# Performance work log

Measured on AMD Instinct MI355X. Metric: run time of the kernel, lower is better.

## Reference

```python
import jax, jax.numpy as jnp
import numpy as np

HIDDEN = 512
INPUT = 512


def setup_inputs() -> dict:
    key = jax.random.key(0)
    ks = jax.random.split(key, 13)
    stdv = 1.0 / np.sqrt(HIDDEN)
    u = lambda k, shape: jax.random.uniform(k, shape, jnp.float32, -stdv, stdv)
    inp = {"x": jax.random.normal(ks[0], (64, 1024, INPUT), jnp.float32)}
    names = ["W_i", "U_i", "b_i", "W_f", "U_f", "b_f", "W_c", "U_c", "b_c", "W_o", "U_o", "b_o"]
    shapes = [(INPUT, HIDDEN), (HIDDEN, HIDDEN), (HIDDEN,)] * 4
    for n, s, k in zip(names, shapes, ks[1:]):
        inp[n] = u(k, s)
    return inp


def reference(x, W_i, U_i, b_i, W_f, U_f, b_f, W_c, U_c, b_c, W_o, U_o, b_o):
    bs, seq, _ = x.shape
    hs = U_i.shape[0]
    # Precompute input projections for all timesteps (batched GEMM), then scan the recurrence.
    # Stack 4 gates: [seq, bs, 4*hs]
    W = jnp.concatenate([W_i, W_f, W_c, W_o], axis=1)          # [in, 4h]
    U = jnp.concatenate([U_i, U_f, U_c, U_o], axis=1)          # [h, 4h]
    b = jnp.concatenate([b_i, b_f, b_c, b_o], axis=0)          # [4h]
    x_proj = jnp.einsum('bsi,ih->sbh', x, W) + b               # [seq, bs, 4h]

    def step(carry, xp):
        h, c = carry
        z = xp + h @ U                                          # [bs, 4h]
        i = jax.nn.relu(z[:, 0*hs:1*hs])
        f = jax.nn.relu(z[:, 1*hs:2*hs])
        g = jnp.tanh(z[:, 2*hs:3*hs])
        o = jax.nn.sigmoid(z[:, 3*hs:4*hs])
        c = f * c + i * g
        h = o * jnp.tanh(c)
        return (h, c), h

    h0 = jnp.zeros((bs, hs), x.dtype)
    c0 = jnp.zeros((bs, hs), x.dtype)
    (_, _), hs_seq = jax.lax.scan(step, (h0, c0), x_proj)       # [seq, bs, h]
    return jnp.transpose(hs_seq, (1, 0, 2))                     # [bs, seq, h]
```

## Files before the change

kernel.cpp:

```cpp
#include <hip/hip_runtime.h>
#include <hip/hip_bf16.h>
#include <stdint.h>

typedef float  f32x4  __attribute__((ext_vector_type(4)));
typedef short  bf16x8 __attribute__((ext_vector_type(8)));
typedef unsigned int  u32;
typedef unsigned short u16;
typedef unsigned long long u64;

#define BS    64
#define SEQ   1024
#define HID   512

__device__ __forceinline__ u16 f2bf(float f) {
    u32 u = __float_as_uint(f);
    u32 r = (u + 0x7FFFu + ((u >> 16) & 1u)) >> 16;
    return (u16)r;
}
__device__ __forceinline__ float bf2f(u16 h) {
    return __uint_as_float(((u32)h) << 16);
}
__device__ __forceinline__ u32 pk2(float a, float b) {
    return (u32)f2bf(a) | ((u32)f2bf(b) << 16);
}
__device__ __forceinline__ float sigm(float x)  { return 1.f / (1.f + __expf(-x)); }
__device__ __forceinline__ float tanh_(float x) { return 1.f - 2.f / (1.f + __expf(2.f * x)); }

#define OFF_W4T   0
#define OFF_B4    (2u*1024*1024)
#define OFF_HBUF  (OFF_B4 + 8192)
#define OFF_CBUF  (OFF_HBUF + 262144)
#define OFF_XP    (4u*1024*1024)

__global__ void pack_w(const float* __restrict__ Wi, const float* __restrict__ Wf,
                       const float* __restrict__ Wc, const float* __restrict__ Wo,
                       const float* __restrict__ bi, const float* __restrict__ bf_,
                       const float* __restrict__ bc, const float* __restrict__ bo,
                       u16* __restrict__ w4t, float* __restrict__ b4) {
    int n = blockIdx.x;
    int gate = n >> 9, c = n & 511;
    const float* W = (gate == 0) ? Wi : (gate == 1) ? Wf : (gate == 2) ? Wc : Wo;
    const float* B = (gate == 0) ? bi : (gate == 1) ? bf_ : (gate == 2) ? bc : bo;
    int k = threadIdx.x * 2;
    u32 v = pk2(W[(size_t)k * 512 + c], W[(size_t)(k + 1) * 512 + c]);
    *(u32*)&w4t[(size_t)n * 512 + k] = v;
    if (threadIdx.x == 0) b4[n] = B[c];
}

__global__ __launch_bounds__(256, 2)
void gemm_proj(const float* __restrict__ x, const u16* __restrict__ w4t,
               const float* __restrict__ b4, u16* __restrict__ xp,
               int t0, int Tc) {
    __shared__ __align__(16) u16 lA[128 * 64];
    __shared__ __align__(16) u16 lB[128 * 64];

    int ntb = blockIdx.x & 15;
    int mb  = blockIdx.x >> 4;
    int tps = Tc >> 7;
    int bstrip = mb / tps, tb = mb % tps;
    const float* Abase = x + (size_t)(bstrip * SEQ + t0 + tb * 128) * 512;
    size_t xprow0 = (size_t)bstrip * Tc + tb * 128;
    int n0 = ntb * 128;

    int tid = threadIdx.x, lane = tid & 63, w = tid >> 6;
    int wm = w >> 1, wn = w & 1;

    f32x4 acc[4][4];
#pragma unroll
    for (int a = 0; a < 4; a++)
#pragma unroll
        for (int b = 0; b < 4; b++) acc[a][b] = (f32x4){0.f, 0.f, 0.f, 0.f};

    for (int kb = 0; kb < 8; kb++) {
        {
            int row = tid >> 1, half = tid & 1;
            const float* src = Abase + (size_t)row * 512 + kb * 64 + half * 32;
            u32 tmp[16];
#pragma unroll
            for (int q = 0; q < 8; q++) {
                float4 f = *(const float4*)(src + q * 4);
                tmp[q * 2]     = pk2(f.x, f.y);
                tmp[q * 2 + 1] = pk2(f.z, f.w);
            }
            u16* dst = &lA[row * 64 + half * 32];
#pragma unroll
            for (int q = 0; q < 4; q++)
                *(uint4*)(dst + q * 8) = *(uint4*)&tmp[q * 4];
        }
        {
            int row = tid >> 1, kc = (tid & 1) * 32;
            const u16* src = w4t + (size_t)(n0 + row) * 512 + kb * 64 + kc;
            uint4 v0 = *(const uint4*)(src);
            uint4 v1 = *(const uint4*)(src + 8);
            uint4 v2 = *(const uint4*)(src + 16);
            uint4 v3 = *(const uint4*)(src + 24);
            u16* dst = &lB[row * 64 + kc];
            *(uint4*)(dst) = v0; *(uint4*)(dst + 8) = v1;
            *(uint4*)(dst + 16) = v2; *(uint4*)(dst + 24) = v3;
        }
        __syncthreads();
#pragma unroll
        for (int kt = 0; kt < 2; kt++) {
            bf16x8 a[4], bb[4];
#pragma unroll
            for (int mt = 0; mt < 4; mt++)
                a[mt] = *(const bf16x8*)&lA[(wm * 64 + mt * 16 + (lane & 15)) * 64 + kt * 32 + (lane >> 4) * 8];
#pragma unroll
            for (int nt = 0; nt < 4; nt++)
                bb[nt] = *(const bf16x8*)&lB[(wn * 64 + nt * 16 + (lane & 15)) * 64 + kt * 32 + (lane >> 4) * 8];
#pragma unroll
            for (int mt = 0; mt < 4; mt++)
#pragma unroll
                for (int nt = 0; nt < 4; nt++)
                    acc[mt][nt] = __builtin_amdgcn_mfma_f32_16x16x32_bf16(a[mt], bb[nt], acc[mt][nt], 0, 0, 0);
        }
        __syncthreads();
    }
#pragma unroll
    for (int nt = 0; nt < 4; nt++) {
        int n = n0 + wn * 64 + nt * 16 + (lane & 15);
        float bv = b4[n];
#pragma unroll
        for (int mt = 0; mt < 4; mt++)
#pragma unroll
            for (int r = 0; r < 4; r++) {
                size_t m = xprow0 + wm * 64 + mt * 16 + (lane >> 4) * 4 + r;
                xp[m * 2048 + n] = f2bf(acc[mt][nt][r] + bv);
            }
    }
}

__global__ __launch_bounds__(256, 1)
void lstm_rec(const float* __restrict__ U0, const float* __restrict__ U1,
              const float* __restrict__ U2, const float* __restrict__ U3,
              const u16* __restrict__ xp, float* __restrict__ out,
              u64* __restrict__ hb, float* __restrict__ cbuf, int t0, int Tc) {
    const int gid = blockIdx.x >> 3;
    const int q   = blockIdx.x & 7;
    const int tid = threadIdx.x;
    const int w = tid >> 6, lane = tid & 63;
    const int col16 = lane & 15;
    const int krow  = lane >> 4;
    const int mycol = q * 64 + w * 16 + col16;

    __shared__ __align__(16) u16 h_lds[2][16 * 512];

    const float* Ug[4] = {U0, U1, U2, U3};
    bf16x8 ub[16][4];
#pragma unroll
    for (int kt = 0; kt < 16; kt++) {
        int kbase = kt * 32 + krow * 8;
#pragma unroll
        for (int g = 0; g < 4; g++) {
            union { u16 sh[8]; bf16x8 v; } uu;
#pragma unroll
            for (int j = 0; j < 8; j++)
                uu.sh[j] = f2bf(Ug[g][(size_t)(kbase + j) * 512 + mycol]);
            ub[kt][g] = uu.v;
        }
    }

    float c[4];
    if (t0 == 0) {
        c[0] = c[1] = c[2] = c[3] = 0.f;
    } else {
#pragma unroll
        for (int r = 0; r < 4; r++)
            c[r] = cbuf[((size_t)gid * 16 + krow * 4 + r) * 512 + mycol];
    }

    for (int tl = 0; tl < Tc; tl++) {
        const int t = t0 + tl;

        u16 xr[4][4];
#pragma unroll
        for (int g = 0; g < 4; g++)
#pragma unroll
            for (int r = 0; r < 4; r++)
                xr[g][r] = xp[(size_t)((gid * 16 + krow * 4 + r) * Tc + tl) * 2048
                              + g * 512 + mycol];

        u32 hp[16];
        {
            const u64* src = hb + (((size_t)((t + 1) & 1)) << 14) + ((size_t)gid << 12) + tid;
            const u32 te = (u32)t & 0xFFFFu;
            for (;;) {
                u64 v[16];
#pragma unroll
                for (int j = 0; j < 16; j++)
                    v[j] = __hip_atomic_load(src + j * 256, __ATOMIC_RELAXED,
                                             __HIP_MEMORY_SCOPE_AGENT);
                u32 ok = 1;
#pragma unroll
                for (int j = 0; j < 16; j++) {
                    u32 w0 = (u32)v[j], w1 = (u32)(v[j] >> 32);
                    ok &= (u32)((w0 & 0xFFFFu) == te) & (u32)((w1 & 0xFFFFu) == te);
                }
                if (ok) {
#pragma unroll
                    for (int j = 0; j < 16; j++)
                        hp[j] = ((u32)v[j] >> 16) | ((u32)(v[j] >> 32) & 0xFFFF0000u);
                    break;
                }
            }
        }

        u16* hl = &h_lds[t & 1][0];
#pragma unroll
        for (int j = 0; j < 16; j++) {
            u32 byte = ((u32)(j * 1024) + (u32)(tid * 4)) ^ ((u32)(j & 7) << 4);
            *(u32*)((char*)hl + byte) = hp[j];
        }
        __syncthreads();

        f32x4 acc[4];
#pragma unroll
        for (int g = 0; g < 4; g++) acc[g] = (f32x4){0.f, 0.f, 0.f, 0.f};
#pragma unroll
        for (int kt = 0; kt < 16; kt++) {
            u32 byte = ((u32)(col16 * 1024) + (u32)(kt * 64) + (u32)(krow * 16))
                       ^ ((u32)(col16 & 7) << 4);
            bf16x8 af = *(const bf16x8*)((const char*)hl + byte);
#pragma unroll
            for (int g = 0; g < 4; g++)
                acc[g] = __builtin_amdgcn_mfma_f32_16x16x32_bf16(af, ub[kt][g], acc[g], 0, 0, 0);
        }

        float hv[4];
#pragma unroll
        for (int r = 0; r < 4; r++) {
            float zi = acc[0][r] + bf2f(xr[0][r]);
            float zf = acc[1][r] + bf2f(xr[1][r]);
            float zg = acc[2][r] + bf2f(xr[2][r]);
            float zo = acc[3][r] + bf2f(xr[3][r]);
            float iv = fmaxf(zi, 0.f), fv = fmaxf(zf, 0.f);
            float gv = tanh_(zg), ov = sigm(zo);
            c[r] = fv * c[r] + iv * gv;
            hv[r] = ov * tanh_(c[r]);
        }

        {
            const u32 tag = (u32)((t + 1) & 0xFFFF);
            u32* dst = (u32*)(hb + (((size_t)(t & 1)) << 14) + ((size_t)gid << 12));
#pragma unroll
            for (int r = 0; r < 4; r++) {
                int row = krow * 4 + r;
                u32 word = ((u32)f2bf(hv[r]) << 16) | tag;
                __hip_atomic_store(dst + row * 512 + mycol, word, __ATOMIC_RELAXED,
                                   __HIP_MEMORY_SCOPE_AGENT);
            }
        }

#pragma unroll
        for (int r = 0; r < 4; r++)
            out[(size_t)((gid * 16 + krow * 4 + r) * SEQ + t) * 512 + mycol] = hv[r];
    }

#pragma unroll
    for (int r = 0; r < 4; r++)
        cbuf[((size_t)gid * 16 + krow * 4 + r) * 512 + mycol] = c[r];
}

extern "C" void kernel_launch(void* const* d_in, const int* in_sizes, int n_in,
                              void* d_out, int out_size, void* d_ws, size_t ws_size,
                              hipStream_t stream) {
    const float* x  = (const float*)d_in[0];
    const float* Wg[4] = {(const float*)d_in[1], (const float*)d_in[4],
                          (const float*)d_in[7], (const float*)d_in[10]};
    const float* Ug[4] = {(const float*)d_in[2], (const float*)d_in[5],
                          (const float*)d_in[8], (const float*)d_in[11]};
    const float* Bg[4] = {(const float*)d_in[3], (const float*)d_in[6],
                          (const float*)d_in[9], (const float*)d_in[12]};
    float* out = (float*)d_out;

    char* ws = (char*)d_ws;
    u16*   w4t   = (u16*)(ws + OFF_W4T);
    float* b4    = (float*)(ws + OFF_B4);
    u64*   hb    = (u64*)(ws + OFF_HBUF);
    float* cbuf  = (float*)(ws + OFF_CBUF);
    u16*   xp    = (u16*)(ws + OFF_XP);

    int Tc = 128;
    for (int c = 1024; c >= 128; c >>= 1)
        if ((size_t)OFF_XP + (size_t)BS * c * 2048 * 2 <= ws_size) { Tc = c; break; }

    hipMemsetAsync(ws + OFF_HBUF, 0, 262144, stream);

    pack_w<<<2048, 256, 0, stream>>>(Wg[0], Wg[1], Wg[2], Wg[3],
                                     Bg[0], Bg[1], Bg[2], Bg[3], w4t, b4);

    for (int t0 = 0; t0 < SEQ; t0 += Tc) {
        dim3 ggrid((unsigned)(BS * (Tc / 128) * 16));
        gemm_proj<<<ggrid, 256, 0, stream>>>(x, w4t, b4, xp, t0, Tc);
        lstm_rec<<<32, 256, 0, stream>>>(Ug[0], Ug[1], Ug[2], Ug[3],
                                         xp, out, hb, cbuf, t0, Tc);
    }
}
```

Baseline: 3.876 ms.

## Transpose h exchange buffer layout and prefetch next-step input projection

Result: slower. 5.462 ms (+40.9%).

```diff
diff --git a/kernel.cpp b/kernel.cpp
--- a/kernel.cpp
+++ b/kernel.cpp
@@ -134,7 +134,7 @@
 void lstm_rec(const float* __restrict__ U0, const float* __restrict__ U1,
               const float* __restrict__ U2, const float* __restrict__ U3,
               const u16* __restrict__ xp, float* __restrict__ out,
-              u64* __restrict__ hb, float* __restrict__ cbuf, int t0, int Tc) {
+              u32* __restrict__ hb, float* __restrict__ cbuf, int t0, int Tc) {
     const int gid = blockIdx.x >> 3;
     const int q   = blockIdx.x & 7;
     const int tid = threadIdx.x;
@@ -169,49 +169,59 @@
             c[r] = cbuf[((size_t)gid * 16 + krow * 4 + r) * 512 + mycol];
     }
 
+    u16 xrc[4][4];
+#pragma unroll
+    for (int g = 0; g < 4; g++)
+#pragma unroll
+        for (int r = 0; r < 4; r++)
+            xrc[g][r] = xp[(size_t)((gid * 16 + krow * 4 + r) * Tc + 0) * 2048
+                           + g * 512 + mycol];
+
     for (int tl = 0; tl < Tc; tl++) {
         const int t = t0 + tl;
 
-        u16 xr[4][4];
-#pragma unroll
-        for (int g = 0; g < 4; g++)
-#pragma unroll
-            for (int r = 0; r < 4; r++)
-                xr[g][r] = xp[(size_t)((gid * 16 + krow * 4 + r) * Tc + tl) * 2048
-                              + g * 512 + mycol];
-
-        u32 hp[16];
-        {
-            const u64* src = hb + (((size_t)((t + 1) & 1)) << 14) + ((size_t)gid << 12) + tid;
+        u64 v[16];
+        {
+            const u64* src = (const u64*)((const char*)hb
+                              + (((size_t)((t + 1) & 1) * 4 + gid) << 15)
+                              + (size_t)tid * 128);
             const u32 te = (u32)t & 0xFFFFu;
             for (;;) {
-                u64 v[16];
 #pragma unroll
                 for (int j = 0; j < 16; j++)
-                    v[j] = __hip_atomic_load(src + j * 256, __ATOMIC_RELAXED,
+                    v[j] = __hip_atomic_load(src + j, __ATOMIC_RELAXED,
                                              __HIP_MEMORY_SCOPE_AGENT);
-                u32 ok = 1;
+                u32 bad = 0;
 #pragma unroll
                 for (int j = 0; j < 16; j++) {
-                    u32 w0 = (u32)v[j], w1 = (u32)(v[j] >> 32);
-                    ok &= (u32)((w0 & 0xFFFFu) == te) & (u32)((w1 & 0xFFFFu) == te);
+                    bad |= (((u32)v[j]) ^ te) & 0xFFFFu;
+                    bad |= (((u32)(v[j] >> 32)) ^ te) & 0xFFFFu;
                 }
-                if (ok) {
-#pragma unroll
-                    for (int j = 0; j < 16; j++)
-                        hp[j] = ((u32)v[j] >> 16) | ((u32)(v[j] >> 32) & 0xFFFF0000u);
-                    break;
-                }
+                if (!bad) break;
             }
         }
 
         u16* hl = &h_lds[t & 1][0];
 #pragma unroll
-        for (int j = 0; j < 16; j++) {
-            u32 byte = ((u32)(j * 1024) + (u32)(tid * 4)) ^ ((u32)(j & 7) << 4);
-            *(u32*)((char*)hl + byte) = hp[j];
+        for (int R = 0; R < 16; R++) {
+            u32 lo = (R & 1) ? (u32)(v[R >> 1] >> 32)       : (u32)v[R >> 1];
+            u32 hi = (R & 1) ? (u32)(v[8 + (R >> 1)] >> 32) : (u32)v[8 + (R >> 1)];
+            u32 packed = (lo >> 16) | (hi & 0xFFFF0000u);
+            u32 byte = ((u32)(R * 1024) + (u32)(tid * 4)) ^ ((u32)(R & 7) << 4);
+            *(u32*)((char*)hl + byte) = packed;
         }
         __syncthreads();
+
+        u16 xrn[4][4];
+        {
+            int tln = (tl + 1 < Tc) ? (tl + 1) : tl;
+#pragma unroll
+            for (int g = 0; g < 4; g++)
+#pragma unroll
+                for (int r = 0; r < 4; r++)
+                    xrn[g][r] = xp[(size_t)((gid * 16 + krow * 4 + r) * Tc + tln) * 2048
+                                   + g * 512 + mycol];
+        }
 
         f32x4 acc[4];
 #pragma unroll
@@ -229,10 +239,10 @@
         float hv[4];
 #pragma unroll
         for (int r = 0; r < 4; r++) {
-            float zi = acc[0][r] + bf2f(xr[0][r]);
-            float zf = acc[1][r] + bf2f(xr[1][r]);
-            float zg = acc[2][r] + bf2f(xr[2][r]);
-            float zo = acc[3][r] + bf2f(xr[3][r]);
+            float zi = acc[0][r] + bf2f(xrc[0][r]);
+            float zf = acc[1][r] + bf2f(xrc[1][r]);
+            float zg = acc[2][r] + bf2f(xrc[2][r]);
+            float zo = acc[3][r] + bf2f(xrc[3][r]);
             float iv = fmaxf(zi, 0.f), fv = fmaxf(zf, 0.f);
             float gv = tanh_(zg), ov = sigm(zo);
             c[r] = fv * c[r] + iv * gv;
@@ -241,19 +251,26 @@
 
         {
             const u32 tag = (u32)((t + 1) & 0xFFFF);
-            u32* dst = (u32*)(hb + (((size_t)(t & 1)) << 14) + ((size_t)gid << 12));
-#pragma unroll
-            for (int r = 0; r < 4; r++) {
-                int row = krow * 4 + r;
-                u32 word = ((u32)f2bf(hv[r]) << 16) | tag;
-                __hip_atomic_store(dst + row * 512 + mycol, word, __ATOMIC_RELAXED,
-                                   __HIP_MEMORY_SCOPE_AGENT);
-            }
+            u32 w0 = ((u32)f2bf(hv[0]) << 16) | tag;
+            u32 w1 = ((u32)f2bf(hv[1]) << 16) | tag;
+            u32 w2 = ((u32)f2bf(hv[2]) << 16) | tag;
+            u32 w3 = ((u32)f2bf(hv[3]) << 16) | tag;
+            u64* dst = (u64*)((char*)hb + (((size_t)(t & 1) * 4 + gid) << 15)
+                              + ((size_t)mycol * 64 + krow * 16));
+            __hip_atomic_store(dst,     (u64)w0 | ((u64)w1 << 32),
+                               __ATOMIC_RELAXED, __HIP_MEMORY_SCOPE_AGENT);
+            __hip_atomic_store(dst + 1, (u64)w2 | ((u64)w3 << 32),
+                               __ATOMIC_RELAXED, __HIP_MEMORY_SCOPE_AGENT);
         }
 
 #pragma unroll
         for (int r = 0; r < 4; r++)
             out[(size_t)((gid * 16 + krow * 4 + r) * SEQ + t) * 512 + mycol] = hv[r];
+
+#pragma unroll
+        for (int g = 0; g < 4; g++)
+#pragma unroll
+            for (int r = 0; r < 4; r++) xrc[g][r] = xrn[g][r];
     }
 
 #pragma unroll
@@ -276,7 +293,7 @@
     char* ws = (char*)d_ws;
     u16*   w4t   = (u16*)(ws + OFF_W4T);
     float* b4    = (float*)(ws + OFF_B4);
-    u64*   hb    = (u64*)(ws + OFF_HBUF);
+    u32*   hb    = (u32*)(ws + OFF_HBUF);
     float* cbuf  = (float*)(ws + OFF_CBUF);
     u16*   xp    = (u16*)(ws + OFF_XP);
 
```

## Interleave two batch groups per block to overlap h-exchange latency with compute

Applied to the files above, without the earlier changes.

New measurement: 6.791 ms. 1.75x slower.

```diff
diff --git a/kernel.cpp b/kernel.cpp
--- a/kernel.cpp
+++ b/kernel.cpp
@@ -28,8 +28,8 @@
 
 #define OFF_W4T   0
 #define OFF_B4    (2u*1024*1024)
-#define OFF_HBUF  (OFF_B4 + 8192)
-#define OFF_CBUF  (OFF_HBUF + 262144)
+#define OFF_HB    (OFF_B4 + 8192)
+#define OFF_CBUF  (OFF_HB + 262144)
 #define OFF_XP    (4u*1024*1024)
 
 __global__ void pack_w(const float* __restrict__ Wi, const float* __restrict__ Wf,
@@ -135,15 +135,16 @@
               const float* __restrict__ U2, const float* __restrict__ U3,
               const u16* __restrict__ xp, float* __restrict__ out,
               u64* __restrict__ hb, float* __restrict__ cbuf, int t0, int Tc) {
-    const int gid = blockIdx.x >> 3;
+    const int pr  = blockIdx.x >> 3;
     const int q   = blockIdx.x & 7;
+    const int cA  = pr * 2, cB = pr * 2 + 1;
     const int tid = threadIdx.x;
     const int w = tid >> 6, lane = tid & 63;
     const int col16 = lane & 15;
     const int krow  = lane >> 4;
     const int mycol = q * 64 + w * 16 + col16;
 
-    __shared__ __align__(16) u16 h_lds[2][16 * 512];
+    __shared__ __align__(16) u16 h_lds[2][2][16 * 512];
 
     const float* Ug[4] = {U0, U1, U2, U3};
     bf16x8 ub[16][4];
@@ -160,105 +161,169 @@
         }
     }
 
-    float c[4];
+    float ccA[4], ccB[4];
     if (t0 == 0) {
-        c[0] = c[1] = c[2] = c[3] = 0.f;
+#pragma unroll
+        for (int r = 0; r < 4; r++) { ccA[r] = 0.f; ccB[r] = 0.f; }
     } else {
 #pragma unroll
-        for (int r = 0; r < 4; r++)
-            c[r] = cbuf[((size_t)gid * 16 + krow * 4 + r) * 512 + mycol];
+        for (int r = 0; r < 4; r++) {
+            ccA[r] = cbuf[((size_t)cA * 16 + krow * 4 + r) * 512 + mycol];
+            ccB[r] = cbuf[((size_t)cB * 16 + krow * 4 + r) * 512 + mycol];
+        }
+    }
+
+    auto read16 = [&](u64* vv, const u64* src) {
+#pragma unroll
+        for (int j = 0; j < 16; j++)
+            vv[j] = __hip_atomic_load(src + j * 256, __ATOMIC_RELAXED,
+                                      __HIP_MEMORY_SCOPE_AGENT);
+    };
+    auto tagsbad = [&](const u64* vv, u32 te) -> u32 {
+        u32 bad = 0;
+#pragma unroll
+        for (int j = 0; j < 16; j++) {
+            bad |= (((u32)vv[j]) ^ te) & 0xFFFFu;
+            bad |= (((u32)(vv[j] >> 32)) ^ te) & 0xFFFFu;
+        }
+        return bad;
+    };
+    auto stage16 = [&](const u64* vv, u16* hl) {
+#pragma unroll
+        for (int j = 0; j < 16; j++) {
+            u32 packed = ((u32)vv[j] >> 16) | ((u32)(vv[j] >> 32) & 0xFFFF0000u);
+            u32 byte = ((u32)(j * 1024) + (u32)(tid * 4)) ^ ((u32)(j & 7) << 4);
+            *(u32*)((char*)hl + byte) = packed;
+        }
+    };
+
+    u64 v[16];
+    {
+        const u64* srcA0 = hb + (((size_t)((t0 + 1) & 1)) << 14) + ((size_t)cA << 12) + tid;
+        read16(v, srcA0);
     }
 
     for (int tl = 0; tl < Tc; tl++) {
         const int t = t0 + tl;
-
-        u16 xr[4][4];
+        const u32 te = (u32)t & 0xFFFFu;
+
+        u16 xrA[4][4], xrB[4][4];
 #pragma unroll
         for (int g = 0; g < 4; g++)
 #pragma unroll
-            for (int r = 0; r < 4; r++)
-                xr[g][r] = xp[(size_t)((gid * 16 + krow * 4 + r) * Tc + tl) * 2048
-                              + g * 512 + mycol];
-
-        u32 hp[16];
-        {
-            const u64* src = hb + (((size_t)((t + 1) & 1)) << 14) + ((size_t)gid << 12) + tid;
-            const u32 te = (u32)t & 0xFFFFu;
-            for (;;) {
-                u64 v[16];
-#pragma unroll
-                for (int j = 0; j < 16; j++)
-                    v[j] = __hip_atomic_load(src + j * 256, __ATOMIC_RELAXED,
-                                             __HIP_MEMORY_SCOPE_AGENT);
-                u32 ok = 1;
-#pragma unroll
-                for (int j = 0; j < 16; j++) {
-                    u32 w0 = (u32)v[j], w1 = (u32)(v[j] >> 32);
-                    ok &= (u32)((w0 & 0xFFFFu) == te) & (u32)((w1 & 0xFFFFu) == te);
-                }
-                if (ok) {
-#pragma unroll
-                    for (int j = 0; j < 16; j++)
-                        hp[j] = ((u32)v[j] >> 16) | ((u32)(v[j] >> 32) & 0xFFFF0000u);
-                    break;
-                }
-            }
-        }
-
-        u16* hl = &h_lds[t & 1][0];
-#pragma unroll
-        for (int j = 0; j < 16; j++) {
-            u32 byte = ((u32)(j * 1024) + (u32)(tid * 4)) ^ ((u32)(j & 7) << 4);
-            *(u32*)((char*)hl + byte) = hp[j];
-        }
+            for (int r = 0; r < 4; r++) {
+                xrA[g][r] = xp[(size_t)((cA * 16 + krow * 4 + r) * Tc + tl) * 2048
+                               + g * 512 + mycol];
+                xrB[g][r] = xp[(size_t)((cB * 16 + krow * 4 + r) * Tc + tl) * 2048
+                               + g * 512 + mycol];
+            }
+
+        const u64* srcA = hb + (((size_t)((t + 1) & 1)) << 14) + ((size_t)cA << 12) + tid;
+        const u64* srcB = hb + (((size_t)((t + 1) & 1)) << 14) + ((size_t)cB << 12) + tid;
+
+        while (tagsbad(v, te)) read16(v, srcA);
+        stage16(v, &h_lds[0][t & 1][0]);
         __syncthreads();
-
-        f32x4 acc[4];
-#pragma unroll
-        for (int g = 0; g < 4; g++) acc[g] = (f32x4){0.f, 0.f, 0.f, 0.f};
-#pragma unroll
-        for (int kt = 0; kt < 16; kt++) {
-            u32 byte = ((u32)(col16 * 1024) + (u32)(kt * 64) + (u32)(krow * 16))
-                       ^ ((u32)(col16 & 7) << 4);
-            bf16x8 af = *(const bf16x8*)((const char*)hl + byte);
-#pragma unroll
-            for (int g = 0; g < 4; g++)
-                acc[g] = __builtin_amdgcn_mfma_f32_16x16x32_bf16(af, ub[kt][g], acc[g], 0, 0, 0);
-        }
-
-        float hv[4];
-#pragma unroll
-        for (int r = 0; r < 4; r++) {
-            float zi = acc[0][r] + bf2f(xr[0][r]);
-            float zf = acc[1][r] + bf2f(xr[1][r]);
-            float zg = acc[2][r] + bf2f(xr[2][r]);
-            float zo = acc[3][r] + bf2f(xr[3][r]);
-            float iv = fmaxf(zi, 0.f), fv = fmaxf(zf, 0.f);
-            float gv = tanh_(zg), ov = sigm(zo);
-            c[r] = fv * c[r] + iv * gv;
-            hv[r] = ov * tanh_(c[r]);
-        }
-
+        read16(v, srcB);
+
+        float hvA[4];
+        {
+            const u16* hl = &h_lds[0][t & 1][0];
+            f32x4 acc[4];
+#pragma unroll
+            for (int g = 0; g < 4; g++) acc[g] = (f32x4){0.f, 0.f, 0.f, 0.f};
+#pragma unroll
+            for (int kt = 0; kt < 16; kt++) {
+                u32 byte = ((u32)(col16 * 1024) + (u32)(kt * 64) + (u32)(krow * 16))
+                           ^ ((u32)(col16 & 7) << 4);
+                bf16x8 af = *(const bf16x8*)((const char*)hl + byte);
+#pragma unroll
+                for (int g = 0; g < 4; g++)
+                    acc[g] = __builtin_amdgcn_mfma_f32_16x16x32_bf16(af, ub[kt][g], acc[g], 0, 0, 0);
+            }
+#pragma unroll
+            for (int r = 0; r < 4; r++) {
+                float zi = acc[0][r] + bf2f(xrA[0][r]);
+                float zf = acc[1][r] + bf2f(xrA[1][r]);
+                float zg = acc[2][r] + bf2f(xrA[2][r]);
+                float zo = acc[3][r] + bf2f(xrA[3][r]);
+                float iv = fmaxf(zi, 0.f), fv = fmaxf(zf, 0.f);
+                float gv = tanh_(zg), ov = sigm(zo);
+                ccA[r] = fv * ccA[r] + iv * gv;
+                hvA[r] = ov * tanh_(ccA[r]);
+            }
+        }
         {
             const u32 tag = (u32)((t + 1) & 0xFFFF);
-            u32* dst = (u32*)(hb + (((size_t)(t & 1)) << 14) + ((size_t)gid << 12));
+            u32* dst = (u32*)(hb + (((size_t)(t & 1) * 4 + cA) << 12));
 #pragma unroll
             for (int r = 0; r < 4; r++) {
                 int row = krow * 4 + r;
-                u32 word = ((u32)f2bf(hv[r]) << 16) | tag;
+                u32 word = ((u32)f2bf(hvA[r]) << 16) | tag;
                 __hip_atomic_store(dst + row * 512 + mycol, word, __ATOMIC_RELAXED,
                                    __HIP_MEMORY_SCOPE_AGENT);
             }
         }
-
 #pragma unroll
         for (int r = 0; r < 4; r++)
-            out[(size_t)((gid * 16 + krow * 4 + r) * SEQ + t) * 512 + mycol] = hv[r];
-    }
-
-#pragma unroll
-    for (int r = 0; r < 4; r++)
-        cbuf[((size_t)gid * 16 + krow * 4 + r) * 512 + mycol] = c[r];
+            out[(size_t)((cA * 16 + krow * 4 + r) * SEQ + t) * 512 + mycol] = hvA[r];
+
+        while (tagsbad(v, te)) read16(v, srcB);
+        stage16(v, &h_lds[1][t & 1][0]);
+        __syncthreads();
+        {
+            const u64* srcA2 = hb + (((size_t)(t & 1)) << 14) + ((size_t)cA << 12) + tid;
+            read16(v, srcA2);
+        }
+
+        float hvB[4];
+        {
+            const u16* hl = &h_lds[1][t & 1][0];
+            f32x4 acc[4];
+#pragma unroll
+            for (int g = 0; g < 4; g++) acc[g] = (f32x4){0.f, 0.f, 0.f, 0.f};
+#pragma unroll
+            for (int kt = 0; kt < 16; kt++) {
+                u32 byte = ((u32)(col16 * 1024) + (u32)(kt * 64) + (u32)(krow * 16))
+                           ^ ((u32)(col16 & 7) << 4);
+                bf16x8 af = *(const bf16x8*)((const char*)hl + byte);
+#pragma unroll
+                for (int g = 0; g < 4; g++)
+                    acc[g] = __builtin_amdgcn_mfma_f32_16x16x32_bf16(af, ub[kt][g], acc[g], 0, 0, 0);
+            }
+#pragma unroll
+            for (int r = 0; r < 4; r++) {
+                float zi = acc[0][r] + bf2f(xrB[0][r]);
+                float zf = acc[1][r] + bf2f(xrB[1][r]);
+                float zg = acc[2][r] + bf2f(xrB[2][r]);
+                float zo = acc[3][r] + bf2f(xrB[3][r]);
+                float iv = fmaxf(zi, 0.f), fv = fmaxf(zf, 0.f);
+                float gv = tanh_(zg), ov = sigm(zo);
+                ccB[r] = fv * ccB[r] + iv * gv;
+                hvB[r] = ov * tanh_(ccB[r]);
+            }
+        }
+        {
+            const u32 tag = (u32)((t + 1) & 0xFFFF);
+            u32* dst = (u32*)(hb + (((size_t)(t & 1) * 4 + cB) << 12));
+#pragma unroll
+            for (int r = 0; r < 4; r++) {
+                int row = krow * 4 + r;
+                u32 word = ((u32)f2bf(hvB[r]) << 16) | tag;
+                __hip_atomic_store(dst + row * 512 + mycol, word, __ATOMIC_RELAXED,
+                                   __HIP_MEMORY_SCOPE_AGENT);
+            }
+        }
+#pragma unroll
+        for (int r = 0; r < 4; r++)
+            out[(size_t)((cB * 16 + krow * 4 + r) * SEQ + t) * 512 + mycol] = hvB[r];
+    }
+
+#pragma unroll
+    for (int r = 0; r < 4; r++) {
+        cbuf[((size_t)cA * 16 + krow * 4 + r) * 512 + mycol] = ccA[r];
+        cbuf[((size_t)cB * 16 + krow * 4 + r) * 512 + mycol] = ccB[r];
+    }
 }
 
 extern "C" void kernel_launch(void* const* d_in, const int* in_sizes, int n_in,
@@ -276,7 +341,7 @@
     char* ws = (char*)d_ws;
     u16*   w4t   = (u16*)(ws + OFF_W4T);
     float* b4    = (float*)(ws + OFF_B4);
-    u64*   hb    = (u64*)(ws + OFF_HBUF);
+    u64*   hb    = (u64*)(ws + OFF_HB);
     float* cbuf  = (float*)(ws + OFF_CBUF);
     u16*   xp    = (u16*)(ws + OFF_XP);
 
@@ -284,7 +349,7 @@
     for (int c = 1024; c >= 128; c >>= 1)
         if ((size_t)OFF_XP + (size_t)BS * c * 2048 * 2 <= ws_size) { Tc = c; break; }
 
-    hipMemsetAsync(ws + OFF_HBUF, 0, 262144, stream);
+    hipMemsetAsync(ws + OFF_HB, 0, 262144, stream);
 
     pack_w<<<2048, 256, 0, stream>>>(Wg[0], Wg[1], Wg[2], Wg[3],
                                      Bg[0], Bg[1], Bg[2], Bg[3], w4t, b4);
@@ -292,7 +357,7 @@
     for (int t0 = 0; t0 < SEQ; t0 += Tc) {
         dim3 ggrid((unsigned)(BS * (Tc / 128) * 16));
         gemm_proj<<<ggrid, 256, 0, stream>>>(x, w4t, b4, xp, t0, Tc);
-        lstm_rec<<<32, 256, 0, stream>>>(Ug[0], Ug[1], Ug[2], Ug[3],
+        lstm_rec<<<16, 256, 0, stream>>>(Ug[0], Ug[1], Ug[2], Ug[3],
                                          xp, out, hb, cbuf, t0, Tc);
     }
 }
```
